# Kernel tuning notes

Hardware: AMD Instinct MI355X
Metric: run time of the kernel (lower is better)

The kernel has to match this reference:

```python
import jax, jax.numpy as jnp
import numpy as np

B = 524288  # batch
NQ = 4      # qubits -> 16-dim state vector


def _rx(t):
    c = jnp.cos(t / 2).astype(jnp.complex64)
    s = (-1j * jnp.sin(t / 2)).astype(jnp.complex64)
    return jnp.stack([jnp.stack([c, s], -1), jnp.stack([s, c], -1)], -2)


def _ry(t):
    c = jnp.cos(t / 2)
    s = jnp.sin(t / 2)
    return jnp.stack([jnp.stack([c, -s], -1), jnp.stack([s, c], -1)], -2).astype(jnp.complex64)


def _rz(t):
    em = jnp.exp(-0.5j * t).astype(jnp.complex64)
    ep = jnp.exp(0.5j * t).astype(jnp.complex64)
    z = jnp.zeros_like(em)
    return jnp.stack([jnp.stack([em, z], -1), jnp.stack([z, ep], -1)], -2)


def _apply(state, U, w):
    # state: [B,2,2,2,2]; wire w lives on axis w+1
    s = jnp.moveaxis(state, w + 1, 1)
    if U.ndim == 3:  # per-sample gate (encoder)
        s = jnp.einsum('bij,bj...->bi...', U, s)
    else:            # shared trainable gate
        s = jnp.einsum('ij,bj...->bi...', U, s)
    return jnp.moveaxis(s, 1, w + 1)


def _cnot(state, c, t):
    s = jnp.moveaxis(state, (c + 1, t + 1), (1, 2))
    s = jnp.stack([s[:, 0], s[:, 1, ::-1]], axis=1)  # flip target where control=1
    return jnp.moveaxis(s, (1, 2), (c + 1, t + 1))


def setup_inputs() -> dict:
    key = jax.random.key(0)
    k1, k2 = jax.random.split(key)
    inputs = jax.random.normal(k1, (B, 4), dtype=jnp.float32)
    theta = jax.random.normal(k2, (16,), dtype=jnp.float32)
    return {"inputs": inputs, "theta": theta}


def reference(inputs, theta):
    b = inputs.shape[0]
    state = jnp.zeros((b, 16), jnp.complex64).at[:, 0].set(1.0)
    state = state.reshape(b, 2, 2, 2, 2)
    # --- encoder: per-sample rotations rx(w0), ry(w1), rz(w2), rx(w3) ---
    state = _apply(state, _rx(inputs[:, 0]), 0)
    state = _apply(state, _ry(inputs[:, 1]), 1)
    state = _apply(state, _rz(inputs[:, 2]), 2)
    state = _apply(state, _rx(inputs[:, 3]), 3)
    # --- trainable 20-op layer (fixed representative sequence) ---
    k = 0
    for q in range(NQ):
        state = _apply(state, _rx(theta[k]), q); k += 1
        state = _apply(state, _ry(theta[k]), q); k += 1
        state = _apply(state, _rz(theta[k]), q); k += 1
    for (c, t) in [(0, 1), (1, 2), (2, 3), (3, 0)]:
        state = _cnot(state, c, t)
    for q in range(NQ):
        state = _apply(state, _rx(theta[k]), q); k += 1
    # --- MeasureAll(PauliZ): <Z_w> per wire ---
    flat = state.reshape(b, 16)
    probs = flat.real ** 2 + flat.imag ** 2  # [B,16]
    bits = (jnp.arange(16)[:, None] >> jnp.arange(NQ - 1, -1, -1)[None, :]) & 1  # [16,4], wire0=MSB
    sign = (1.0 - 2.0 * bits).astype(jnp.float32)
    expz = probs @ sign  # [B,4]
    return expz[:, :, None]  # unsqueeze(-1)
```

## Files before the change

kernel.cpp:

```cpp
#include <hip/hip_runtime.h>


__global__ __launch_bounds__(256) void qsim_kernel(
        const float* __restrict__ x,
        const float* __restrict__ theta,
        float* __restrict__ out,
        int n) {
    __shared__ __align__(16) float cst[40];
    int tid = threadIdx.x;
    if (tid < 4) {
        int q = tid;
        float a = theta[3*q], bb = theta[3*q+1], c = theta[3*q+2];
        float sa, ca, sb, cb, sc, cc;
        __sincosf(0.5f*a,  &sa, &ca);
        __sincosf(0.5f*bb, &sb, &cb);
        __sincosf(0.5f*c,  &sc, &cc);
        float m00r =  cb*ca, m00i =  sb*sa;
        float m01r = -sb*ca, m01i = -cb*sa;
        float m10r =  sb*ca, m10i = -cb*sa;
        float m11r =  cb*ca, m11i = -sb*sa;
        float* Tq = cst + 8*q;
        Tq[0] = cc*m00r + sc*m00i;  Tq[1] = cc*m00i - sc*m00r;
        Tq[2] = cc*m01r + sc*m01i;  Tq[3] = cc*m01i - sc*m01r;
        Tq[4] = cc*m10r - sc*m10i;  Tq[5] = cc*m10i + sc*m10r;
        Tq[6] = cc*m11r - sc*m11i;  Tq[7] = cc*m11i + sc*m11r;
        float sfq, cfq;
        __sincosf(theta[12+q], &sfq, &cfq);
        cst[32+q] = cfq;
        cst[36+q] = (q == 3 ? -8.0f : 4.0f) * sfq;
    }
    __syncthreads();

    int b = blockIdx.x * 256 + tid;
    if (b >= n) return;

    float4 xv = ((const float4*)x)[b];

    float T[32];
    #pragma unroll
    for (int i = 0; i < 8; ++i) ((float4*)T)[i] = ((const float4*)cst)[i];
    float4 cf = ((const float4*)cst)[8];
    float4 sf = ((const float4*)cst)[9];

    float s0 = __sinf(0.5f*xv.x), c0 = __cosf(0.5f*xv.x);
    float s1 = __sinf(0.5f*xv.y), c1 = __cosf(0.5f*xv.y);
    float s2 = __sinf(0.5f*xv.z), c2 = __cosf(0.5f*xv.z);
    float s3 = __sinf(0.5f*xv.w), c3 = __cosf(0.5f*xv.w);

    float var[4], vai[4], vbr[4], vbi[4];
    {
        const float* t = T + 0;
        var[0] = t[0]*c0 + t[3]*s0;  vai[0] = t[1]*c0 - t[2]*s0;
        vbr[0] = t[4]*c0 + t[7]*s0;  vbi[0] = t[5]*c0 - t[6]*s0;
    }
    {
        const float* t = T + 8;
        var[1] = t[0]*c1 + t[2]*s1;  vai[1] = t[1]*c1 + t[3]*s1;
        vbr[1] = t[4]*c1 + t[6]*s1;  vbi[1] = t[5]*c1 + t[7]*s1;
    }
    {
        const float* t = T + 16;
        var[2] = t[0]*c2 + t[1]*s2;  vai[2] = t[1]*c2 - t[0]*s2;
        vbr[2] = t[4]*c2 + t[5]*s2;  vbi[2] = t[5]*c2 - t[4]*s2;
    }
    {
        const float* t = T + 24;
        var[3] = t[0]*c3 + t[3]*s3;  vai[3] = t[1]*c3 - t[2]*s3;
        vbr[3] = t[4]*c3 + t[7]*s3;  vbi[3] = t[5]*c3 - t[6]*s3;
    }

    float zq[4], Xq[4], Yq[4];
    #pragma unroll
    for (int w = 0; w < 4; ++w) {
        float p0 = var[w]*var[w] + vai[w]*vai[w];
        float p1 = vbr[w]*vbr[w] + vbi[w]*vbi[w];
        zq[w] = p0 - p1;
        Xq[w] = var[w]*vbr[w] + vai[w]*vbi[w];
        Yq[w] = var[w]*vbi[w] - vai[w]*vbr[w];
    }

    float z01 = zq[0]*zq[1];
    float z23 = zq[2]*zq[3];
    float4 o;
    o.x = (cf.x*zq[1] + sf.x*(Xq[0]*Yq[1])) * z23;
    o.y = (cf.y*zq[1] + sf.y*(Yq[1]*Xq[2])) * zq[0];
    o.z = (cf.z*zq[2] + sf.z*(Yq[2]*Xq[3])) * z01;
    o.w = cf.w*(z01*z23) + sf.w*((Yq[0]*Yq[1])*(zq[2]*Yq[3]));
    ((float4*)out)[b] = o;
}

extern "C" void kernel_launch(void* const* d_in, const int* in_sizes, int n_in,
                              void* d_out, int out_size, void* d_ws, size_t ws_size,
                              hipStream_t stream) {
    const float* inputs = (const float*)d_in[0];
    const float* theta  = (const float*)d_in[1];
    float* out = (float*)d_out;
    int n = in_sizes[0] / 4;
    int blocks = (n + 255) / 256;
    qsim_kernel<<<blocks, 256, 0, stream>>>(inputs, theta, out, n);
}
```

Baseline: 62.73 us.

## Fold per-wire Bloch-vector algebra into precomputed constants and drop wire-2 math

Rewrites the per-sample math in Bloch-vector form: each encoded wire's Z/X/Y components become linear in cos/sin of the full input angle, using constants precomputed per block. The wire-2 input is eliminated because an RZ encoder gate does not change Z expectations, so its sin/cos are no longer computed. The x load is also moved ahead of the shared-memory setup and barrier so global latency overlaps with it, using a clamped index. The intent is fewer ALU ops and transcendentals per thread in this memory-bound kernel; it relies on the algebraic identities being exactly right.

```diff
diff --git a/kernel.cpp b/kernel.cpp
--- a/kernel.cpp
+++ b/kernel.cpp
@@ -6,86 +6,74 @@
         const float* __restrict__ theta,
         float* __restrict__ out,
         int n) {
-    __shared__ __align__(16) float cst[40];
+    __shared__ __align__(16) float cst[32];
     int tid = threadIdx.x;
+    int b = blockIdx.x * 256 + tid;
+
+    float4 xv = ((const float4*)x)[min(b, n - 1)];
+
     if (tid < 4) {
         int q = tid;
-        float a = theta[3*q], bb = theta[3*q+1], c = theta[3*q+2];
         float sa, ca, sb, cb, sc, cc;
-        __sincosf(0.5f*a,  &sa, &ca);
-        __sincosf(0.5f*bb, &sb, &cb);
-        __sincosf(0.5f*c,  &sc, &cc);
-        float m00r =  cb*ca, m00i =  sb*sa;
-        float m01r = -sb*ca, m01i = -cb*sa;
-        float m10r =  sb*ca, m10i = -cb*sa;
-        float m11r =  cb*ca, m11i = -sb*sa;
-        float* Tq = cst + 8*q;
-        Tq[0] = cc*m00r + sc*m00i;  Tq[1] = cc*m00i - sc*m00r;
-        Tq[2] = cc*m01r + sc*m01i;  Tq[3] = cc*m01i - sc*m01r;
-        Tq[4] = cc*m10r - sc*m10i;  Tq[5] = cc*m10i + sc*m10r;
-        Tq[6] = cc*m11r - sc*m11i;  Tq[7] = cc*m11i + sc*m11r;
-        float sfq, cfq;
-        __sincosf(theta[12+q], &sfq, &cfq);
-        cst[32+q] = cfq;
-        cst[36+q] = (q == 3 ? -8.0f : 4.0f) * sfq;
+        __sincosf(theta[3*q],   &sa, &ca);
+        __sincosf(theta[3*q+1], &sb, &cb);
+        __sincosf(theta[3*q+2], &sc, &cc);
+        float sa2, ca2, sb2, cb2, sc2, cc2;
+        __sincosf(theta[6], &sa2, &ca2);
+        __sincosf(theta[7], &sb2, &cb2);
+        __sincosf(theta[8], &sc2, &cc2);
+        float X2c = cc2*sb2*ca2 + sc2*sa2;
+        float Y2c = sc2*sb2*ca2 - cc2*sa2;
+        float Z2c = cb2*ca2;
+        float sf, cf;
+        __sincosf(theta[12+q], &sf, &cf);
+        float A, Bc;
+        if (q == 0)      { A = cf*Z2c; Bc =  sf*Z2c; }
+        else if (q == 1) { A = cf;     Bc =  sf*X2c; }
+        else if (q == 2) { A = cf*Z2c; Bc =  sf*Y2c; }
+        else             { A = cf*Z2c; Bc = -sf*Z2c; }
+        cst[24+q] = A; cst[28+q] = Bc;
+        if (q == 0) {
+            cst[0]=cc*sb*sa - sc*ca; cst[1]=sc*sb*sa + cc*ca; cst[2]=cb*sa; cst[3]=0.f;
+            cst[4]=cc*sb*ca + sc*sa; cst[5]=sc*sb*ca - cc*sa; cst[6]=cb*ca; cst[7]=0.f;
+        } else if (q == 1) {
+            cst[8]=cc*cb;  cst[9]=sc*cb; cst[10]=-sb; cst[11]=0.f;
+            cst[12]=cc*sb*ca + sc*sa; cst[13]=sc*sb*ca - cc*sa; cst[14]=cb*ca; cst[15]=0.f;
+        } else if (q == 3) {
+            cst[16]=cc*sb*sa - sc*ca; cst[17]=sc*sb*sa + cc*ca; cst[18]=cb*sa; cst[19]=0.f;
+            cst[20]=cc*sb*ca + sc*sa; cst[21]=sc*sb*ca - cc*sa; cst[22]=cb*ca; cst[23]=0.f;
+        }
     }
     __syncthreads();
 
-    int b = blockIdx.x * 256 + tid;
     if (b >= n) return;
 
-    float4 xv = ((const float4*)x)[b];
+    float C[32];
+    #pragma unroll
+    for (int i = 0; i < 8; ++i) ((float4*)C)[i] = ((const float4*)cst)[i];
 
-    float T[32];
-    #pragma unroll
-    for (int i = 0; i < 8; ++i) ((float4*)T)[i] = ((const float4*)cst)[i];
-    float4 cf = ((const float4*)cst)[8];
-    float4 sf = ((const float4*)cst)[9];
+    float s0 = __sinf(xv.x), c0 = __cosf(xv.x);
+    float s1 = __sinf(xv.y), c1 = __cosf(xv.y);
+    float s3 = __sinf(xv.w), c3 = __cosf(xv.w);
 
-    float s0 = __sinf(0.5f*xv.x), c0 = __cosf(0.5f*xv.x);
-    float s1 = __sinf(0.5f*xv.y), c1 = __cosf(0.5f*xv.y);
-    float s2 = __sinf(0.5f*xv.z), c2 = __cosf(0.5f*xv.z);
-    float s3 = __sinf(0.5f*xv.w), c3 = __cosf(0.5f*xv.w);
+    float X0 = c0*C[4]  - s0*C[0];
+    float Y0 = c0*C[5]  - s0*C[1];
+    float z0 = c0*C[6]  - s0*C[2];
+    float Y1 = s1*C[9]  + c1*C[13];
+    float z1 = s1*C[10] + c1*C[14];
+    float X3 = c3*C[20] - s3*C[16];
+    float Y3 = c3*C[21] - s3*C[17];
+    float z3 = c3*C[22] - s3*C[18];
 
-    float var[4], vai[4], vbr[4], vbi[4];
-    {
-        const float* t = T + 0;
-        var[0] = t[0]*c0 + t[3]*s0;  vai[0] = t[1]*c0 - t[2]*s0;
-        vbr[0] = t[4]*c0 + t[7]*s0;  vbi[0] = t[5]*c0 - t[6]*s0;
-    }
-    {
-        const float* t = T + 8;
-        var[1] = t[0]*c1 + t[2]*s1;  vai[1] = t[1]*c1 + t[3]*s1;
-        vbr[1] = t[4]*c1 + t[6]*s1;  vbi[1] = t[5]*c1 + t[7]*s1;
-    }
-    {
-        const float* t = T + 16;
-        var[2] = t[0]*c2 + t[1]*s2;  vai[2] = t[1]*c2 - t[0]*s2;
-        vbr[2] = t[4]*c2 + t[5]*s2;  vbi[2] = t[5]*c2 - t[4]*s2;
-    }
-    {
-        const float* t = T + 24;
-        var[3] = t[0]*c3 + t[3]*s3;  vai[3] = t[1]*c3 - t[2]*s3;
-        vbr[3] = t[4]*c3 + t[7]*s3;  vbi[3] = t[5]*c3 - t[6]*s3;
-    }
+    float A0=C[24], A1=C[25], A2=C[26], A3=C[27];
+    float B0=C[28], B1=C[29], B2=C[30], B3=C[31];
 
-    float zq[4], Xq[4], Yq[4];
-    #pragma unroll
-    for (int w = 0; w < 4; ++w) {
-        float p0 = var[w]*var[w] + vai[w]*vai[w];
-        float p1 = vbr[w]*vbr[w] + vbi[w]*vbi[w];
-        zq[w] = p0 - p1;
-        Xq[w] = var[w]*vbr[w] + vai[w]*vbi[w];
-        Yq[w] = var[w]*vbi[w] - vai[w]*vbr[w];
-    }
-
-    float z01 = zq[0]*zq[1];
-    float z23 = zq[2]*zq[3];
+    float z01 = z0*z1;
     float4 o;
-    o.x = (cf.x*zq[1] + sf.x*(Xq[0]*Yq[1])) * z23;
-    o.y = (cf.y*zq[1] + sf.y*(Yq[1]*Xq[2])) * zq[0];
-    o.z = (cf.z*zq[2] + sf.z*(Yq[2]*Xq[3])) * z01;
-    o.w = cf.w*(z01*z23) + sf.w*((Yq[0]*Yq[1])*(zq[2]*Yq[3]));
+    o.x = z3*(A0*z1 + B0*(X0*Y1));
+    o.y = z0*(A1*z1 + B1*Y1);
+    o.z = z01*(A2 + B2*X3);
+    o.w = A3*(z01*z3) + B3*((Y0*Y1)*Y3);
     ((float4*)out)[b] = o;
 }
 
```

New measurement: 62.05 us. No clear change (-1.1%).
